# Optimization experiments

Hardware: AMD Instinct MI355X
Metric: run time of the kernel (lower is better)

The kernel has to match this reference:

```python
import jax, jax.numpy as jnp
import numpy as np

IN_FEATURES = 4096
OUT_FEATURES = 4096
SPARSITY = 0.99
NNZ = max(int(IN_FEATURES * OUT_FEATURES * (1.0 - SPARSITY)), 1)  # 167772
BATCH = 1024


def setup_inputs() -> dict:
    key = jax.random.key(0)
    kx, kv, kr, kc = jax.random.split(key, 4)
    x = jax.random.normal(kx, (BATCH, IN_FEATURES), dtype=jnp.float32)
    # values initialized ~ N(0,1) / sqrt(in_features), as in the module
    values = jax.random.normal(kv, (NNZ,), dtype=jnp.float32) * (1.0 / np.sqrt(IN_FEATURES))
    bias = jnp.zeros((OUT_FEATURES,), dtype=jnp.float32)
    rows = jax.random.randint(kr, (NNZ,), 0, IN_FEATURES)
    cols = jax.random.randint(kc, (NNZ,), 0, OUT_FEATURES)
    return {"x": x, "values": values, "bias": bias, "rows": rows, "cols": cols}


def reference(x, values, bias, rows, cols):
    # out = x @ W + bias, with sparse W(in,out) given in COO form.
    # torch's coalesce() sums duplicate (row,col) entries; scatter-add matches that.
    contrib = x[:, rows] * values  # [B, nnz]: gather input columns, scale by weights
    out = jnp.zeros((x.shape[0], OUT_FEATURES), dtype=x.dtype)
    out = out.at[:, cols].add(contrib)  # scatter-add into output columns
    return out + bias[None, :]
```

## Files before the change

### kernel.cpp

```cpp
#include <hip/hip_runtime.h>
#include <hip/hip_fp16.h>

#define BATCH 1024
#define IN_F 4096
#define OUT_F 4096
#define NCHUNK 8
#define CHUNK (BATCH / NCHUNK)
#define CAP 128
#define TBLK ((IN_F / 32) * (BATCH / 32))

__global__ __launch_bounds__(256) void prep_k(const float* __restrict__ src,
                                              __half* __restrict__ dst,
                                              const int* __restrict__ rows,
                                              const int* __restrict__ cols,
                                              const float* __restrict__ vals,
                                              int nnz, int nscat,
                                              int* __restrict__ cursor,
                                              int2* __restrict__ rv) {
    const int tid = threadIdx.x;
    if ((int)blockIdx.x < nscat) {
        int k = blockIdx.x * 256 + tid;
        if (k < nnz) {
            int c = cols[k];
            int pos = atomicAdd(&cursor[c], 1);
            if (pos < CAP)
                rv[(size_t)c * CAP + pos] = make_int2(rows[k], __float_as_int(vals[k]));
        }
        return;
    }
    __shared__ float tile[32][33];
    const int b = blockIdx.x - nscat;
    const int bx = b & (IN_F / 32 - 1);
    const int by = b >> 7;
    const int tx = tid & 31, ty = tid >> 5;
    const int c0 = bx * 32, r0 = by * 32;
#pragma unroll
    for (int j = 0; j < 4; ++j) {
        int r = r0 + ty + j * 8;
        tile[ty + j * 8][tx] = src[(size_t)r * IN_F + c0 + tx];
    }
    __syncthreads();
#pragma unroll
    for (int j = 0; j < 4; ++j) {
        int c = c0 + ty + j * 8;
        dst[(size_t)c * BATCH + r0 + tx] = __float2half(tile[tx][ty + j * 8]);
    }
}

__device__ inline void fma8(float acc[8], uint4 h, float v) {
    union { unsigned u; __half2 h2; } cv;
    float2 f;
    cv.u = h.x; f = __half22float2(cv.h2);
    acc[0] = fmaf(v, f.x, acc[0]); acc[1] = fmaf(v, f.y, acc[1]);
    cv.u = h.y; f = __half22float2(cv.h2);
    acc[2] = fmaf(v, f.x, acc[2]); acc[3] = fmaf(v, f.y, acc[3]);
    cv.u = h.z; f = __half22float2(cv.h2);
    acc[4] = fmaf(v, f.x, acc[4]); acc[5] = fmaf(v, f.y, acc[5]);
    cv.u = h.w; f = __half22float2(cv.h2);
    acc[6] = fmaf(v, f.x, acc[6]); acc[7] = fmaf(v, f.y, acc[7]);
}

__global__ __launch_bounds__(256, 4) void spmm_k(const __half* __restrict__ xTh,
                                                 const int* __restrict__ cursor,
                                                 const int2* __restrict__ rv,
                                                 const float* __restrict__ bias,
                                                 float* __restrict__ out) {
    __shared__ float red[4][128];
    const int chunk = blockIdx.x & (NCHUNK - 1);
    const int colBase = (blockIdx.x >> 3) * 4;
    const int w = threadIdx.x >> 6;
    const int lane = threadIdx.x & 63;
    const int q = lane >> 4;
    const int ql = lane & 15;
    const int c = __builtin_amdgcn_readfirstlane(colBase + w);

    int cnt = cursor[c];
    cnt = cnt > CAP ? CAP : cnt;
    const int gfull = cnt >> 3;
    const int rem = cnt & 7;

    const char* __restrict__ xbase =
        (const char*)xTh + chunk * (CHUNK * 2) + ql * 16;
    const int4* __restrict__ pq = (const int4*)(rv + (size_t)c * CAP) + q;

    float acc[8] = {0, 0, 0, 0, 0, 0, 0, 0};

    int4 e0 = pq[0];
    uint4 hA = *(const uint4*)(xbase + ((size_t)(e0.x & (IN_F - 1)) << 11));
    uint4 hB = *(const uint4*)(xbase + ((size_t)(e0.z & (IN_F - 1)) << 11));
    int4 e1 = pq[4];

#pragma unroll 2
    for (int g = 0; g < gfull; ++g) {
        int4 e2 = pq[(size_t)(g + 2) * 4];
        uint4 hA1 = *(const uint4*)(xbase + ((size_t)(e1.x & (IN_F - 1)) << 11));
        uint4 hB1 = *(const uint4*)(xbase + ((size_t)(e1.z & (IN_F - 1)) << 11));
        fma8(acc, hA, __int_as_float(e0.y));
        fma8(acc, hB, __int_as_float(e0.w));
        e0 = e1; e1 = e2; hA = hA1; hB = hB1;
    }
    if (rem) {
        const int i0 = gfull * 8 + 2 * q;
        float vA = (i0 < cnt) ? __int_as_float(e0.y) : 0.0f;
        float vB = (i0 + 1 < cnt) ? __int_as_float(e0.w) : 0.0f;
        fma8(acc, hA, vA);
        fma8(acc, hB, vB);
    }

#pragma unroll
    for (int j = 0; j < 8; ++j) {
        acc[j] += __shfl_xor(acc[j], 16);
        acc[j] += __shfl_xor(acc[j], 32);
    }

    if (q == 0) {
        *(float4*)&red[w][ql * 8 + 0] = make_float4(acc[0], acc[1], acc[2], acc[3]);
        *(float4*)&red[w][ql * 8 + 4] = make_float4(acc[4], acc[5], acc[6], acc[7]);
    }
    __syncthreads();

    const int t = threadIdx.x;
    if (t < 128) {
        float4 o;
        o.x = red[0][t] + bias[colBase + 0];
        o.y = red[1][t] + bias[colBase + 1];
        o.z = red[2][t] + bias[colBase + 2];
        o.w = red[3][t] + bias[colBase + 3];
        *(float4*)(out + (size_t)(chunk * CHUNK + t) * OUT_F + colBase) = o;
    }
}

__global__ void bias_init_k(const float* __restrict__ bias, float* __restrict__ out) {
    int i = blockIdx.x * 256 + threadIdx.x;
    out[i] = bias[i & (OUT_F - 1)];
}
__global__ void fallback_k(const float* __restrict__ x, const float* __restrict__ vals,
                           const int* __restrict__ rows, const int* __restrict__ cols,
                           float* __restrict__ out) {
    int k = blockIdx.x;
    int r = rows[k], c = cols[k];
    float v = vals[k];
    for (int b = threadIdx.x; b < BATCH; b += 256)
        atomicAdd(&out[(size_t)b * OUT_F + c], v * x[(size_t)b * IN_F + r]);
}

extern "C" void kernel_launch(void* const* d_in, const int* in_sizes, int n_in,
                              void* d_out, int out_size, void* d_ws, size_t ws_size,
                              hipStream_t stream) {
    const float* x    = (const float*)d_in[0];
    const float* vals = (const float*)d_in[1];
    const float* bias = (const float*)d_in[2];
    const int*   rows = (const int*)d_in[3];
    const int*   cols = (const int*)d_in[4];
    float* out = (float*)d_out;
    const int nnz = in_sizes[1];

    const size_t rv_bytes = (size_t)OUT_F * CAP * 8 + 256;

    size_t off = 0;
    auto alloc = [&](size_t bytes) {
        void* p = (char*)d_ws + off;
        off += (bytes + 255) & ~(size_t)255;
        return p;
    };
    __half* xTh   = (__half*)alloc((size_t)IN_F * BATCH * 2);
    int*   cursor = (int*)alloc(OUT_F * 4);
    int2*  rv     = (int2*)alloc(rv_bytes);

    if (off > ws_size) {
        bias_init_k<<<(BATCH * OUT_F) / 256, 256, 0, stream>>>(bias, out);
        fallback_k<<<nnz, 256, 0, stream>>>(x, vals, rows, cols, out);
        return;
    }

    const int nscat = (nnz + 255) / 256;
    hipMemsetAsync(cursor, 0, OUT_F * sizeof(int), stream);
    prep_k<<<nscat + TBLK, 256, 0, stream>>>(x, xTh, rows, cols, vals, nnz, nscat,
                                             cursor, rv);
    spmm_k<<<(OUT_F / 4) * NCHUNK, 256, 0, stream>>>(xTh, cursor, rv, bias, out);
}
```

Before: 112.6 us.

## Remap spmm lanes: whole wave walks all nnz per batch chunk, 4 halves per lane

Changes the work split in the sparse kernel. Each wave used to divide a column's nonzeros across four lane groups and reduce them with shuffles. Now every lane walks all nonzeros of the column and gathers 4 halves (8 bytes) over a 256-row batch chunk, and the number of batch chunks drops from 8 to 4. This removes the cross-lane shuffle reduction and halves the number of times the COO list is re-read across chunks. In exchange the gathers are narrower, each lane runs a longer serial chain of loads and FMAs, there is less memory-level parallelism per lane, and the grid has fewer blocks.

```diff
diff --git a/kernel.cpp b/kernel.cpp
--- a/kernel.cpp
+++ b/kernel.cpp
@@ -4,7 +4,7 @@
 #define BATCH 1024
 #define IN_F 4096
 #define OUT_F 4096
-#define NCHUNK 8
+#define NCHUNK 4
 #define CHUNK (BATCH / NCHUNK)
 #define CAP 128
 #define TBLK ((IN_F / 32) * (BATCH / 32))
@@ -47,17 +47,23 @@
     }
 }
 
-__device__ inline void fma8(float acc[8], uint4 h, float v) {
+__device__ inline void fma4(float acc[4], uint2 h, float v) {
     union { unsigned u; __half2 h2; } cv;
     float2 f;
     cv.u = h.x; f = __half22float2(cv.h2);
     acc[0] = fmaf(v, f.x, acc[0]); acc[1] = fmaf(v, f.y, acc[1]);
     cv.u = h.y; f = __half22float2(cv.h2);
     acc[2] = fmaf(v, f.x, acc[2]); acc[3] = fmaf(v, f.y, acc[3]);
-    cv.u = h.z; f = __half22float2(cv.h2);
-    acc[4] = fmaf(v, f.x, acc[4]); acc[5] = fmaf(v, f.y, acc[5]);
-    cv.u = h.w; f = __half22float2(cv.h2);
-    acc[6] = fmaf(v, f.x, acc[6]); acc[7] = fmaf(v, f.y, acc[7]);
+}
+
+__device__ inline void gfma(float acc[4], const char* xb, int row, float v) {
+    uint2 h = *(const uint2*)(xb + ((size_t)(row & (IN_F - 1)) << 11));
+    fma4(acc, h, v);
+}
+
+__device__ inline void ldround(int4 d[4], const int4* __restrict__ pq, int r) {
+#pragma unroll
+    for (int i = 0; i < 4; ++i) d[i] = pq[r * 4 + i];
 }
 
 __global__ __launch_bounds__(256, 4) void spmm_k(const __half* __restrict__ xTh,
@@ -65,69 +71,61 @@
                                                  const int2* __restrict__ rv,
                                                  const float* __restrict__ bias,
                                                  float* __restrict__ out) {
-    __shared__ float red[4][128];
+    __shared__ float red[4][CHUNK];
     const int chunk = blockIdx.x & (NCHUNK - 1);
-    const int colBase = (blockIdx.x >> 3) * 4;
+    const int colBase = (blockIdx.x >> 2) * 4;
     const int w = threadIdx.x >> 6;
     const int lane = threadIdx.x & 63;
-    const int q = lane >> 4;
-    const int ql = lane & 15;
     const int c = __builtin_amdgcn_readfirstlane(colBase + w);
 
+    const int4* __restrict__ pq = (const int4*)(rv + (size_t)c * CAP);
+    const char* xb = (const char*)xTh + chunk * (CHUNK * 2) + lane * 8;
+
+    int4 s0[4], s1[4], s2[4];
+    ldround(s0, pq, 0);
+    ldround(s1, pq, 1);
     int cnt = cursor[c];
     cnt = cnt > CAP ? CAP : cnt;
     const int gfull = cnt >> 3;
     const int rem = cnt & 7;
 
-    const char* __restrict__ xbase =
-        (const char*)xTh + chunk * (CHUNK * 2) + ql * 16;
-    const int4* __restrict__ pq = (const int4*)(rv + (size_t)c * CAP) + q;
-
-    float acc[8] = {0, 0, 0, 0, 0, 0, 0, 0};
-
-    int4 e0 = pq[0];
-    uint4 hA = *(const uint4*)(xbase + ((size_t)(e0.x & (IN_F - 1)) << 11));
-    uint4 hB = *(const uint4*)(xbase + ((size_t)(e0.z & (IN_F - 1)) << 11));
-    int4 e1 = pq[4];
+    float acc[4] = {0.f, 0.f, 0.f, 0.f};
 
 #pragma unroll 2
-    for (int g = 0; g < gfull; ++g) {
-        int4 e2 = pq[(size_t)(g + 2) * 4];
-        uint4 hA1 = *(const uint4*)(xbase + ((size_t)(e1.x & (IN_F - 1)) << 11));
-        uint4 hB1 = *(const uint4*)(xbase + ((size_t)(e1.z & (IN_F - 1)) << 11));
-        fma8(acc, hA, __int_as_float(e0.y));
-        fma8(acc, hB, __int_as_float(e0.w));
-        e0 = e1; e1 = e2; hA = hA1; hB = hB1;
+    for (int r = 0; r < gfull; ++r) {
+        ldround(s2, pq, r + 2);
+        gfma(acc, xb, s0[0].x, __int_as_float(s0[0].y));
+        gfma(acc, xb, s0[0].z, __int_as_float(s0[0].w));
+        gfma(acc, xb, s0[1].x, __int_as_float(s0[1].y));
+        gfma(acc, xb, s0[1].z, __int_as_float(s0[1].w));
+        gfma(acc, xb, s0[2].x, __int_as_float(s0[2].y));
+        gfma(acc, xb, s0[2].z, __int_as_float(s0[2].w));
+        gfma(acc, xb, s0[3].x, __int_as_float(s0[3].y));
+        gfma(acc, xb, s0[3].z, __int_as_float(s0[3].w));
+#pragma unroll
+        for (int i = 0; i < 4; ++i) { s0[i] = s1[i]; s1[i] = s2[i]; }
     }
     if (rem) {
-        const int i0 = gfull * 8 + 2 * q;
-        float vA = (i0 < cnt) ? __int_as_float(e0.y) : 0.0f;
-        float vB = (i0 + 1 < cnt) ? __int_as_float(e0.w) : 0.0f;
-        fma8(acc, hA, vA);
-        fma8(acc, hB, vB);
+        const int b0 = gfull * 8;
+        gfma(acc, xb, s0[0].x, (b0 + 0 < cnt) ? __int_as_float(s0[0].y) : 0.f);
+        gfma(acc, xb, s0[0].z, (b0 + 1 < cnt) ? __int_as_float(s0[0].w) : 0.f);
+        gfma(acc, xb, s0[1].x, (b0 + 2 < cnt) ? __int_as_float(s0[1].y) : 0.f);
+        gfma(acc, xb, s0[1].z, (b0 + 3 < cnt) ? __int_as_float(s0[1].w) : 0.f);
+        gfma(acc, xb, s0[2].x, (b0 + 4 < cnt) ? __int_as_float(s0[2].y) : 0.f);
+        gfma(acc, xb, s0[2].z, (b0 + 5 < cnt) ? __int_as_float(s0[2].w) : 0.f);
+        gfma(acc, xb, s0[3].x, (b0 + 6 < cnt) ? __int_as_float(s0[3].y) : 0.f);
+        gfma(acc, xb, s0[3].z, (b0 + 7 < cnt) ? __int_as_float(s0[3].w) : 0.f);
     }
 
-#pragma unroll
-    for (int j = 0; j < 8; ++j) {
-        acc[j] += __shfl_xor(acc[j], 16);
-        acc[j] += __shfl_xor(acc[j], 32);
-    }
-
-    if (q == 0) {
-        *(float4*)&red[w][ql * 8 + 0] = make_float4(acc[0], acc[1], acc[2], acc[3]);
-        *(float4*)&red[w][ql * 8 + 4] = make_float4(acc[4], acc[5], acc[6], acc[7]);
-    }
+    *(float4*)&red[w][lane * 4] = make_float4(acc[0], acc[1], acc[2], acc[3]);
     __syncthreads();
-
     const int t = threadIdx.x;
-    if (t < 128) {
-        float4 o;
-        o.x = red[0][t] + bias[colBase + 0];
-        o.y = red[1][t] + bias[colBase + 1];
-        o.z = red[2][t] + bias[colBase + 2];
-        o.w = red[3][t] + bias[colBase + 3];
-        *(float4*)(out + (size_t)(chunk * CHUNK + t) * OUT_F + colBase) = o;
-    }
+    float4 o;
+    o.x = red[0][t] + bias[colBase + 0];
+    o.y = red[1][t] + bias[colBase + 1];
+    o.z = red[2][t] + bias[colBase + 2];
+    o.w = red[3][t] + bias[colBase + 3];
+    *(float4*)(out + (size_t)(chunk * CHUNK + t) * OUT_F + colBase) = o;
 }
 
 __global__ void bias_init_k(const float* __restrict__ bias, float* __restrict__ out) {
```

New measurement: 120.3 us. +6.8%, slower.
